# Optimization experiments

Measured on AMD Instinct MI355X. Metric: run time of the kernel, lower is better.

## Reference

```python
import jax, jax.numpy as jnp
import numpy as np

HID = 512; HH = HID // 2; INP = 1; OUT = 1
INH = int(HID * 0.3); EXC = HID - INH            # 153 / 359
N = 3 * HH + 2 * HID + INP                       # 1793 total units
ALM_EXC_START = 3 * HH + HID                      # start of ALM excitatory block
T_CONST = 0.1; SIGMA_REC = 0.01
B, T = 128, 300


def _np_masks():
    rng = np.random.default_rng(0)
    n_zeros = int(np.ceil(0.9 * HH))
    sparse = np.ones((HH, HH), np.float32)
    for c in range(HH):
        sparse[rng.permutation(HH)[:n_zeros], c] = 0.0
    alm2str = np.concatenate([np.ones((HH, EXC), np.float32), np.zeros((HH, INH), np.float32)], 1)
    thal2d1 = np.concatenate([np.ones((HH // 2, HID), np.float32), np.zeros((HH // 2, HID), np.float32)], 0)
    alm2d1 = 1.0 - thal2d1
    iti2d1 = np.concatenate([np.ones((HH // 2, INP), np.float32), np.zeros((HH // 2, INP), np.float32)], 0)
    alm_sign = np.concatenate([np.ones(EXC, np.float32), -np.ones(INH, np.float32)])  # alm2alm_D diagonal
    return sparse, alm2str, thal2d1, alm2d1, iti2d1, alm_sign

_SPARSE, _ALM2STR, _THAL2D1M, _ALM2D1M, _ITI2D1M, _ALMSIGN = [jnp.asarray(a) for a in _np_masks()]


def _clip(w):
    return jnp.clip(w, 1e-10, 1.0)               # F.hardtanh(w, 1e-10, 1)


def _build_W(d12d1_w, d12d2_w, d22d1_w, d22d2_w, d22stn_w, d12thal_w, stn2thal_w,
             thal2alm_w, alm2alm_w, thal2d1_w, thal2d2_w, alm2d1_w, alm2d2_w,
             inp_w_d1, inp_w_d2):
    z_ss = jnp.zeros((HH, HH)); z_sl = jnp.zeros((HH, HID))
    z_ls = jnp.zeros((HID, HH)); z_ll = jnp.zeros((HID, HID))
    z_si = jnp.zeros((HH, INP)); z_li = jnp.zeros((HID, INP))
    # striatal recurrence: sparse_mask * hardtanh(w) @ (-I)
    d12d1 = -(_SPARSE * _clip(d12d1_w)); d12d2 = -(_SPARSE * _clip(d12d2_w))
    d22d1 = -(_SPARSE * _clip(d22d1_w)); d22d2 = -(_SPARSE * _clip(d22d2_w))
    row_d1 = jnp.concatenate([d12d1, d22d1, z_ss, _THAL2D1M * _clip(thal2d1_w),
                              _ALM2D1M * _ALM2STR * _clip(alm2d1_w), _ITI2D1M * _clip(inp_w_d1)], 1)
    row_d2 = jnp.concatenate([d12d2, d22d2, z_ss, _clip(thal2d2_w),
                              _ALM2STR * _clip(alm2d2_w), _clip(inp_w_d2)], 1)
    row_stn = jnp.concatenate([z_ss, _clip(d22stn_w), z_ss, z_sl, z_sl, z_si], 1)
    row_thal = jnp.concatenate([_clip(d12thal_w), z_ls, -_clip(stn2thal_w), z_ll, z_ll, z_li], 1)  # stn2thal @ (-I)
    row_alm = jnp.concatenate([z_ls, z_ls, z_ls, _clip(thal2alm_w),
                               _clip(alm2alm_w) * _ALMSIGN[None, :], z_li], 1)      # alm2alm @ D (Dale)
    row_iti = jnp.zeros((INP, N))
    return jnp.concatenate([row_d1, row_d2, row_stn, row_thal, row_alm, row_iti], 0)


def setup_inputs() -> dict:
    key = jax.random.key(0)
    ks = jax.random.split(key, 24)
    u = lambda k, s: jax.random.uniform(k, s, jnp.float32) * 0.01   # uniform(0, 0.01) init
    return {
        "inp": jax.random.uniform(ks[0], (B, T, INP), jnp.float32),
        "cue_inp": jax.random.uniform(ks[1], (B, T, INP), jnp.float32),
        "inhib_stim": jnp.zeros((B, T, N), jnp.float32),
        "hn": jax.random.uniform(ks[2], (1, B, N), jnp.float32),
        "xn": jax.random.uniform(ks[3], (1, B, N), jnp.float32),
        "noise": jax.random.normal(ks[4], (B, T, N), jnp.float32),
        "d12d1_w": u(ks[5], (HH, HH)), "d12d2_w": u(ks[6], (HH, HH)),
        "d22d1_w": u(ks[7], (HH, HH)), "d22d2_w": u(ks[8], (HH, HH)),
        "d22stn_w": u(ks[9], (HH, HH)), "d12thal_w": u(ks[10], (HID, HH)),
        "stn2thal_w": u(ks[11], (HID, HH)), "thal2alm_w": u(ks[12], (HID, HID)),
        "alm2alm_w": u(ks[13], (HID, HID)), "thal2d1_w": u(ks[14], (HH, HID)),
        "thal2d2_w": u(ks[15], (HH, HID)), "alm2d1_w": u(ks[16], (HH, HID)),
        "alm2d2_w": u(ks[17], (HH, HID)), "inp_w_d1": u(ks[18], (HH, INP)),
        "inp_w_d2": u(ks[19], (HH, INP)), "out_w_alm": u(ks[20], (OUT, EXC)),
    }


def reference(inp, cue_inp, inhib_stim, hn, xn, noise,
              d12d1_w, d12d2_w, d22d1_w, d22d2_w, d22stn_w, d12thal_w, stn2thal_w,
              thal2alm_w, alm2alm_w, thal2d1_w, thal2d2_w, alm2d1_w, alm2d2_w,
              inp_w_d1, inp_w_d2, out_w_alm):
    W = _build_W(d12d1_w, d12d2_w, d22d1_w, d22d2_w, d22stn_w, d12thal_w, stn2thal_w,
                 thal2alm_w, alm2alm_w, thal2d1_w, thal2d2_w, alm2d1_w, alm2d2_w,
                 inp_w_d1, inp_w_d2)
    # tonic current: 0.1 everywhere except ITI units
    tonic = jnp.concatenate([0.1 * jnp.ones(N - INP, jnp.float32), jnp.zeros(INP, jnp.float32)])
    seq = (inhib_stim.swapaxes(0, 1),                 # [T, B, N]
           (inp + cue_inp).swapaxes(0, 1),            # [T, B, INP] -> injected into ITI units
           noise.swapaxes(0, 1))                      # [T, B, N]

    def step(carry, s):
        x, h = carry
        inh_t, iti_t, noise_t = s
        drive = h @ W.T + tonic + inh_t + SIGMA_REC * noise_t
        drive = drive.at[:, N - INP:].add(iti_t)
        x = x + T_CONST * (-x + drive)
        h = jax.nn.relu(x)
        out = h[:, ALM_EXC_START:ALM_EXC_START + EXC] @ out_w_alm.T
        return (x, h), (h, x, out)

    (_, _), (hs, xs, outs) = jax.lax.scan(step, (xn[0], hn[0]), seq)
    return hs.swapaxes(0, 1), xs.swapaxes(0, 1), outs.swapaxes(0, 1)
```

## Files before the change

### kernel.cpp

```cpp
#include <hip/hip_runtime.h>
#include <stdint.h>
#include <string.h>

#define NREAL 1793
#define NPAD  1824
#define NROWP 1808
#define WSTR  1832
#define NBLK  113
#define NGRP  2
#define TSTEPS 300
#define BATCH 128
#define XS_OFF 68851200
#define OUT_OFF 137702400
#define LOFF (16 * WSTR)
#define LOSCALE 4096.0f
#define LOINV  2.44140625e-4f

#define ASLOT(g,i)    (((g) * 128 + (i)) * 32)

typedef _Float16 half_t;
typedef __attribute__((ext_vector_type(8))) _Float16 half8;
typedef __attribute__((ext_vector_type(4))) float f32x4;
typedef __attribute__((ext_vector_type(4))) unsigned int uint4v;

__device__ __forceinline__ float clipw(float w) {
  return fminf(fmaxf(w, 1e-10f), 1.0f);
}

__device__ __forceinline__ void store_u32_llc(unsigned int* p, unsigned int v) {
  asm volatile("global_store_dword %0, %1, off sc0 sc1"
               :: "v"((unsigned long long)(uintptr_t)p), "v"(v)
               : "memory");
}

__device__ __forceinline__ float unpack_h(uint32_t p) {
  unsigned short uh = (unsigned short)(p & 0xffffu);
  unsigned short ul = (unsigned short)(p >> 16);
  half_t hh = *(half_t*)&uh;
  half_t hl = *(half_t*)&ul;
  return (float)hh + LOINV * (float)hl;
}

template<int LO0, int N0, int LO1, int N1, int LO2, int N2>
__device__ __forceinline__ void seg_mfma(const uint32_t* __restrict__ ap,
                                         const half_t* __restrict__ Wl, int wl_b,
                                         f32x4& acc0, f32x4& acc1, f32x4& acc2)
{
  constexpr int NC = N0 + N1 + N2;
  if (NC == 0) return;
  uint4v q0[NC ? NC : 1], q1[NC ? NC : 1];
  #pragma unroll
  for (int i = 0; i < NC; ++i) {
    const int kc = (i < N0) ? (LO0 + i)
                 : (i < N0 + N1) ? (LO1 + i - N0)
                 : (LO2 + i - N0 - N1);
    q0[i] = *(const uint4v*)(ap + kc * 32);
    q1[i] = *(const uint4v*)(ap + kc * 32 + 4);
  }
  #pragma unroll
  for (int i = 0; i < NC; ++i) {
    const int kc = (i < N0) ? (LO0 + i)
                 : (i < N0 + N1) ? (LO1 + i - N0)
                 : (LO2 + i - N0 - N1);
    uint4v uh, ul;
    uh.x = __builtin_amdgcn_perm(q0[i].y, q0[i].x, 0x05040100u);
    uh.y = __builtin_amdgcn_perm(q0[i].w, q0[i].z, 0x05040100u);
    uh.z = __builtin_amdgcn_perm(q1[i].y, q1[i].x, 0x05040100u);
    uh.w = __builtin_amdgcn_perm(q1[i].w, q1[i].z, 0x05040100u);
    ul.x = __builtin_amdgcn_perm(q0[i].y, q0[i].x, 0x07060302u);
    ul.y = __builtin_amdgcn_perm(q0[i].w, q0[i].z, 0x07060302u);
    ul.z = __builtin_amdgcn_perm(q1[i].y, q1[i].x, 0x07060302u);
    ul.w = __builtin_amdgcn_perm(q1[i].w, q1[i].z, 0x07060302u);
    union { uint4v u; half8 h; } ch, cl;
    ch.u = uh; cl.u = ul;
    half8 bvh = *(const half8*)&Wl[wl_b + kc * 32];
    half8 bvl = *(const half8*)&Wl[LOFF + wl_b + kc * 32];
    acc0 = __builtin_amdgcn_mfma_f32_16x16x32_f16(ch.h, bvh, acc0, 0, 0, 0);
    acc1 = __builtin_amdgcn_mfma_f32_16x16x32_f16(ch.h, bvl, acc1, 0, 0, 0);
    acc2 = __builtin_amdgcn_mfma_f32_16x16x32_f16(cl.h, bvh, acc2, 0, 0, 0);
  }
}

__global__ __launch_bounds__(256)
void build_w(const float* __restrict__ d12d1, const float* __restrict__ d12d2,
             const float* __restrict__ d22d1, const float* __restrict__ d22d2,
             const float* __restrict__ d22stn, const float* __restrict__ d12thal,
             const float* __restrict__ stn2thal, const float* __restrict__ thal2alm,
             const float* __restrict__ alm2alm, const float* __restrict__ thal2d1,
             const float* __restrict__ thal2d2, const float* __restrict__ alm2d1,
             const float* __restrict__ alm2d2, const float* __restrict__ inpw1,
             const float* __restrict__ inpw2, const unsigned int* __restrict__ mbits,
             half_t* __restrict__ W)
{
  int idx = blockIdx.x * 256 + threadIdx.x;
  if (idx >= NROWP * NPAD) return;
  int i = idx / NPAD, j = idx - (idx / NPAD) * NPAD;
  float v = 0.f;
  if (i < NREAL && j < NREAL) {
    if (i < 256) {
      if (j < 512) {
        int jj = j & 255;
        unsigned bit = (mbits[(i << 3) + (jj >> 5)] >> (jj & 31)) & 1u;
        float wv = (j < 256) ? d12d1[(i << 8) + jj] : d22d1[(i << 8) + jj];
        v = bit ? -clipw(wv) : 0.f;
      } else if (j < 768) {
      } else if (j < 1280) {
        if (i < 128) v = clipw(thal2d1[(i << 9) + (j - 768)]);
      } else if (j < 1792) {
        int jj = j - 1280;
        if (i >= 128 && jj < 359) v = clipw(alm2d1[(i << 9) + jj]);
      } else {
        if (i < 128) v = clipw(inpw1[i]);
      }
    } else if (i < 512) {
      int ii = i - 256;
      if (j < 512) {
        int jj = j & 255;
        unsigned bit = (mbits[(ii << 3) + (jj >> 5)] >> (jj & 31)) & 1u;
        float wv = (j < 256) ? d12d2[(ii << 8) + jj] : d22d2[(ii << 8) + jj];
        v = bit ? -clipw(wv) : 0.f;
      } else if (j < 768) {
      } else if (j < 1280) {
        v = clipw(thal2d2[(ii << 9) + (j - 768)]);
      } else if (j < 1792) {
        int jj = j - 1280;
        if (jj < 359) v = clipw(alm2d2[(ii << 9) + jj]);
      } else {
        v = clipw(inpw2[ii]);
      }
    } else if (i < 768) {
      int ii = i - 512;
      if (j >= 256 && j < 512) v = clipw(d22stn[(ii << 8) + (j - 256)]);
    } else if (i < 1280) {
      int ii = i - 768;
      if (j < 256) v = clipw(d12thal[(ii << 8) + j]);
      else if (j >= 512 && j < 768) v = -clipw(stn2thal[(ii << 8) + (j - 512)]);
    } else if (i < 1792) {
      int ii = i - 1280;
      if (j >= 768 && j < 1280) v = clipw(thal2alm[(ii << 9) + (j - 768)]);
      else if (j >= 1280) {
        int jj = j - 1280;
        v = clipw(alm2alm[(ii << 9) + jj]) * ((jj < 359) ? 1.f : -1.f);
      }
    }
  }
  half_t vh = (half_t)v;
  half_t vl = (half_t)((v - (float)vh) * LOSCALE);
  W[idx] = vh;
  W[(size_t)NROWP * NPAD + idx] = vl;
}

__global__ __launch_bounds__(256)
void init_h(const float* __restrict__ hn, uint32_t* __restrict__ hbuf)
{
  const size_t P4 = (size_t)BATCH * NPAD;
  int idx = blockIdx.x * 256 + threadIdx.x;
  if (idx >= BATCH * NPAD) return;
  int b = idx / NPAD, k = idx - b * NPAD;
  float v = (k < NREAL) ? hn[b * NREAL + k] : 0.f;
  half_t vh = (half_t)v;
  half_t vl = (half_t)((v - (float)vh) * LOSCALE);
  uint32_t hp = (uint32_t)(*(unsigned short*)&vh) |
                ((uint32_t)(*(unsigned short*)&vl) << 16);
  hbuf[idx]      = hp;
  hbuf[P4 + idx] = 0u;
}

__global__ __launch_bounds__(256, 1)
void rnn_step_all(const half_t* __restrict__ Wg, uint32_t* __restrict__ hbuf,
                  unsigned int* __restrict__ cnt,
                  const float* __restrict__ inp, const float* __restrict__ cue,
                  const float* __restrict__ inhib, const float* __restrict__ noise,
                  const float* __restrict__ xn, const float* __restrict__ outw,
                  float* __restrict__ dout)
{
  __shared__ __align__(16) half_t Wl[2 * 16 * WSTR];
  const int tid = threadIdx.x;
  const int bid = blockIdx.x;
  const int g  = bid / NBLK;
  const int nb = bid - g * NBLK;
  const int r0 = nb * 16;
  const int bg = g * 64;
  const size_t P4 = (size_t)BATCH * NPAD;

  const int lane = tid & 63;
  const int w    = tid >> 6;
  const int n_i  = lane & 15;
  const int kq   = lane >> 4;
  const int row  = r0 + n_i;
  const bool valid = row < NREAL;
  const int b0 = bg + 16 * w + kq * 4;
  const int bA = bg + 16 * w + n_i;
  const int wl_b = n_i * WSTR + kq * 8;
  const bool is_outblk = (r0 == 512);
  const bool poll_wave = (tid < 64);

  float inh[4], noi[4];
  #pragma unroll
  for (int r = 0; r < 4; ++r) {
    inh[r] = 0.f; noi[r] = 0.f;
    if (valid) {
      int ei = ((b0 + r) * TSTEPS) * NREAL + row;
      inh[r] = __builtin_nontemporal_load(&inhib[ei]);
      noi[r] = __builtin_nontemporal_load(&noise[ei]);
    }
  }

  for (int idx = tid; idx < 2 * 16 * (NPAD / 8); idx += 256) {
    int p   = idx / (16 * (NPAD / 8));
    int rem = idx - p * 16 * (NPAD / 8);
    int rr  = rem / (NPAD / 8);
    int cc  = (rem - rr * (NPAD / 8)) * 8;
    *(uint4v*)&Wl[p * LOFF + rr * WSTR + cc] =
        *(const uint4v*)&Wg[(size_t)p * NROWP * NPAD + (size_t)(r0 + rr) * NPAD + cc];
  }
  __syncthreads();

  float xr[4];
  #pragma unroll
  for (int r = 0; r < 4; ++r)
    xr[r] = valid ? xn[(size_t)(b0 + r) * NREAL + row] : 0.f;

  const float tonic = (valid && row < 1792) ? 0.1f : 0.f;
  const bool is_iti = (row == 1792);

  const int ob    = bg + 16 * w + (lane >> 2);
  const int opart = lane & 3;
  const int ou0   = opart * 90;
  const int onu   = (opart == 3) ? 89 : 90;

  #pragma unroll 1
  for (int t = 0; t < TSTEPS; ++t) {
    const uint32_t* hr = hbuf + (size_t)(t & 1) * P4;
    uint32_t*       hw = hbuf + (size_t)((t & 1) ^ 1) * P4;

    float itv[4];
    #pragma unroll
    for (int r = 0; r < 4; ++r) {
      int bt = (b0 + r) * TSTEPS + t;
      itv[r] = is_iti ? (inp[bt] + cue[bt]) : 0.f;
    }

    const uint32_t* ap = hr + (size_t)bA * NPAD + kq * 8;
    f32x4 acc0 = {0.f, 0.f, 0.f, 0.f};
    f32x4 acc1 = {0.f, 0.f, 0.f, 0.f};
    f32x4 acc2 = {0.f, 0.f, 0.f, 0.f};

    if      (r0 < 128)  seg_mfma<0, 16, 24, 16, 56, 1>(ap, Wl, wl_b, acc0, acc1, acc2);
    else if (r0 < 256)  seg_mfma<0, 16, 40, 12,  0, 0>(ap, Wl, wl_b, acc0, acc1, acc2);
    else if (r0 < 512)  seg_mfma<0, 16, 24, 28, 56, 1>(ap, Wl, wl_b, acc0, acc1, acc2);
    else if (r0 < 768)  seg_mfma<8,  8,  0,  0,  0, 0>(ap, Wl, wl_b, acc0, acc1, acc2);
    else if (r0 < 1280) seg_mfma<0,  8, 16,  8,  0, 0>(ap, Wl, wl_b, acc0, acc1, acc2);
    else if (r0 < 1792) seg_mfma<24, 32, 0,  0,  0, 0>(ap, Wl, wl_b, acc0, acc1, acc2);

    #pragma unroll
    for (int r = 0; r < 4; ++r) {
      float drive = acc0[r] + LOINV * (acc1[r] + acc2[r])
                    + tonic + inh[r] + 0.01f * noi[r] + itv[r];
      float xv = xr[r] + 0.1f * (drive - xr[r]);
      float hv = fmaxf(xv, 0.f);
      xr[r] = xv;
      int bt = (b0 + r) * TSTEPS + t;
      if (valid) {
        int ei = bt * NREAL + row;
        __builtin_nontemporal_store(hv, &dout[ei]);
        __builtin_nontemporal_store(xv, &dout[XS_OFF + ei]);
      }
      half_t hh = (half_t)hv;
      half_t hl = (half_t)((hv - (float)hh) * LOSCALE);
      uint32_t hp = (uint32_t)(*(unsigned short*)&hh) |
                    ((uint32_t)(*(unsigned short*)&hl) << 16);
      store_u32_llc(&hw[(size_t)(b0 + r) * NPAD + row], hp);
    }

    if (is_outblk && t >= 1) {
      const uint32_t* hb = hr + (size_t)ob * NPAD + 1280 + ou0;
      float s = 0.f;
      #pragma unroll 10
      for (int i = 0; i < onu; ++i)
        s += unpack_h(hb[i]) * outw[ou0 + i];
      s += __shfl_xor(s, 1);
      s += __shfl_xor(s, 2);
      if (opart == 0)
        __builtin_nontemporal_store(s, &dout[OUT_OFF + ob * TSTEPS + (t - 1)]);
    }

    if (t + 1 < TSTEPS) {
      #pragma unroll
      for (int r = 0; r < 4; ++r) {
        if (valid) {
          int ei = ((b0 + r) * TSTEPS + (t + 1)) * NREAL + row;
          inh[r] = __builtin_nontemporal_load(&inhib[ei]);
          noi[r] = __builtin_nontemporal_load(&noise[ei]);
        }
      }
      const unsigned epoch = (unsigned)(t + 1);
      asm volatile("s_waitcnt vmcnt(8)" ::: "memory");
      __builtin_amdgcn_s_barrier();
      if (tid == 0)
        store_u32_llc(&cnt[ASLOT(g, nb)], epoch);
      if (poll_wave) {
        unsigned m;
        for (;;) {
          unsigned v0 = __hip_atomic_load(&cnt[ASLOT(g, lane)],
                                          __ATOMIC_RELAXED, __HIP_MEMORY_SCOPE_AGENT);
          unsigned v1 = 0xFFFFFFFFu;
          if (lane + 64 < NBLK)
            v1 = __hip_atomic_load(&cnt[ASLOT(g, lane + 64)],
                                   __ATOMIC_RELAXED, __HIP_MEMORY_SCOPE_AGENT);
          m = v0 < v1 ? v0 : v1;
          #pragma unroll
          for (int o = 32; o; o >>= 1) {
            unsigned mo = __shfl_xor(m, o);
            m = m < mo ? m : mo;
          }
          if (m >= epoch) break;
          __builtin_amdgcn_s_sleep(1);
        }
        __builtin_amdgcn_fence(__ATOMIC_ACQUIRE, "agent");
        asm volatile("s_waitcnt vmcnt(0)" ::: "memory");
      }
      __builtin_amdgcn_s_barrier();
    }
  }

  asm volatile("s_waitcnt vmcnt(0)" ::: "memory");
  __builtin_amdgcn_s_barrier();
  if (tid == 0)
    store_u32_llc(&cnt[ASLOT(g, nb)], (unsigned)TSTEPS);
  if (is_outblk) {
    if (poll_wave) {
      unsigned m;
      for (;;) {
        unsigned v0 = __hip_atomic_load(&cnt[ASLOT(g, lane)],
                                        __ATOMIC_RELAXED, __HIP_MEMORY_SCOPE_AGENT);
        unsigned v1 = 0xFFFFFFFFu;
        if (lane + 64 < NBLK)
          v1 = __hip_atomic_load(&cnt[ASLOT(g, lane + 64)],
                                 __ATOMIC_RELAXED, __HIP_MEMORY_SCOPE_AGENT);
        m = v0 < v1 ? v0 : v1;
        #pragma unroll
        for (int o = 32; o; o >>= 1) {
          unsigned mo = __shfl_xor(m, o);
          m = m < mo ? m : mo;
        }
        if (m >= (unsigned)TSTEPS) break;
        __builtin_amdgcn_s_sleep(1);
      }
      __builtin_amdgcn_fence(__ATOMIC_ACQUIRE, "agent");
      asm volatile("s_waitcnt vmcnt(0)" ::: "memory");
    }
    __builtin_amdgcn_s_barrier();
    const uint32_t* hr = hbuf + (size_t)(TSTEPS & 1) * P4;
    const uint32_t* hb = hr + (size_t)ob * NPAD + 1280 + ou0;
    float s = 0.f;
    #pragma unroll 10
    for (int i = 0; i < onu; ++i)
      s += unpack_h(hb[i]) * outw[ou0 + i];
    s += __shfl_xor(s, 1);
    s += __shfl_xor(s, 2);
    if (opart == 0)
      __builtin_nontemporal_store(s, &dout[OUT_OFF + ob * TSTEPS + (TSTEPS - 1)]);
  }
}

static void compute_sparse_mask(uint32_t* mb) {
  uint32_t pool[4];
  uint32_t hc = 0x43b0d7e5u;
  auto hashmix = [&hc](uint32_t value) -> uint32_t {
    value ^= hc; hc *= 0x931e8875u; value *= hc; value ^= value >> 16; return value;
  };
  auto mixf = [](uint32_t x, uint32_t y) -> uint32_t {
    uint32_t r = x * 0xca01f9ddu;
    r -= y * 0x4973f715u;
    r ^= r >> 16;
    return r;
  };
  for (int i = 0; i < 4; ++i) pool[i] = hashmix(0u);
  for (int s = 0; s < 4; ++s)
    for (int d = 0; d < 4; ++d)
      if (s != d) pool[d] = mixf(pool[d], hashmix(pool[s]));
  uint32_t st[8];
  uint32_t hb = 0x8b51f9ddu;
  for (int i = 0; i < 8; ++i) {
    uint32_t dv = pool[i & 3];
    dv ^= hb; hb *= 0x58f38dedu; dv *= hb; dv ^= dv >> 16;
    st[i] = dv;
  }
  uint64_t v64[4];
  for (int i = 0; i < 4; ++i) v64[i] = (uint64_t)st[2 * i] | ((uint64_t)st[2 * i + 1] << 32);
  typedef unsigned __int128 u128;
  const u128 MULT = ((u128)0x2360ed051fc65da4ULL << 64) | 0x4385df649fccf645ULL;
  u128 initstate = ((u128)v64[0] << 64) | v64[1];
  u128 initseq   = ((u128)v64[2] << 64) | v64[3];
  u128 state = 0, inc = (initseq << 1) | 1;
  state = state * MULT + inc;
  state += initstate;
  state = state * MULT + inc;
  bool has32 = false; uint32_t cached = 0;
  auto next64 = [&]() -> uint64_t {
    state = state * MULT + inc;
    uint64_t hi = (uint64_t)(state >> 64), lo = (uint64_t)state;
    unsigned rot = (unsigned)(state >> 122);
    uint64_t x = hi ^ lo;
    return (x >> rot) | (x << ((64 - rot) & 63));
  };
  auto next32 = [&]() -> uint32_t {
    if (has32) { has32 = false; return cached; }
    uint64_t v = next64();
    has32 = true; cached = (uint32_t)(v >> 32);
    return (uint32_t)v;
  };
  auto rinterval = [&](uint32_t mx) -> uint32_t {
    if (mx == 0) return 0;
    uint32_t mask = mx;
    mask |= mask >> 1; mask |= mask >> 2; mask |= mask >> 4;
    mask |= mask >> 8; mask |= mask >> 16;
    uint32_t value;
    do { value = next32() & mask; } while (value > mx);
    return value;
  };
  for (int i = 0; i < 256 * 8; ++i) mb[i] = 0xFFFFFFFFu;
  int perm[256];
  for (int c = 0; c < 256; ++c) {
    for (int i = 0; i < 256; ++i) perm[i] = i;
    for (int i = 255; i >= 1; --i) {
      uint32_t j = rinterval((uint32_t)i);
      int tmp = perm[i]; perm[i] = perm[j]; perm[j] = tmp;
    }
    for (int z = 0; z < 231; ++z)
      mb[perm[z] * 8 + (c >> 5)] &= ~(1u << (c & 31));
  }
}

extern "C" void kernel_launch(void* const* d_in, const int* in_sizes, int n_in,
                              void* d_out, int out_size, void* d_ws, size_t ws_size,
                              hipStream_t stream)
{
  (void)in_sizes; (void)n_in; (void)out_size; (void)ws_size;
  const float* inp   = (const float*)d_in[0];
  const float* cue   = (const float*)d_in[1];
  const float* inhib = (const float*)d_in[2];
  const float* hn    = (const float*)d_in[3];
  const float* xn    = (const float*)d_in[4];
  const float* noise = (const float*)d_in[5];
  const float* outw  = (const float*)d_in[21];
  float* dout = (float*)d_out;

  char* ws = (char*)d_ws;
  const size_t W_BYTES = (size_t)2 * NROWP * NPAD * sizeof(half_t);
  const size_t H_BYTES = (size_t)2 * BATCH * NPAD * 4;
  half_t*   W    = (half_t*)ws;
  uint32_t* hbuf = (uint32_t*)(ws + W_BYTES);
  unsigned int* mbits = (unsigned int*)(ws + W_BYTES + H_BYTES);
  unsigned int* cnt   = (unsigned int*)(ws + W_BYTES + H_BYTES + 32768);

  static uint32_t hmask[256 * 8];
  compute_sparse_mask(hmask);
  (void)hipMemcpyAsync(mbits, hmask, sizeof(hmask), hipMemcpyHostToDevice, stream);
  (void)hipMemsetAsync(cnt, 0, 32768, stream);

  build_w<<<(NROWP * NPAD + 255) / 256, 256, 0, stream>>>(
      (const float*)d_in[6],  (const float*)d_in[7],  (const float*)d_in[8],
      (const float*)d_in[9],  (const float*)d_in[10], (const float*)d_in[11],
      (const float*)d_in[12], (const float*)d_in[13], (const float*)d_in[14],
      (const float*)d_in[15], (const float*)d_in[16], (const float*)d_in[17],
      (const float*)d_in[18], (const float*)d_in[19], (const float*)d_in[20],
      mbits, W);
  init_h<<<(BATCH * NPAD + 255) / 256, 256, 0, stream>>>(hn, hbuf);

  void* args[] = {(void*)&W, (void*)&hbuf, (void*)&cnt, (void*)&inp, (void*)&cue,
                  (void*)&inhib, (void*)&noise, (void*)&xn, (void*)&outw, (void*)&dout};
  hipError_t err = hipLaunchCooperativeKernel(reinterpret_cast<void*>(rnn_step_all),
                                              dim3(NGRP * NBLK), dim3(256), args, 0, stream);
  if (err != hipSuccess) {
    rnn_step_all<<<dim3(NGRP * NBLK), dim3(256), 0, stream>>>(
        W, hbuf, cnt, inp, cue, inhib, noise, xn, outw, dout);
  }
}
```

Measured before the change: 4.143 ms.

## Replace global per-step barrier with dependency-aware point-to-point waits and quad buffering

Each block now waits only on the row-region blocks whose outputs its sparse weight segments actually read. It also waits on consumers being at most two steps behind, rather than on all blocks in the group every step. The h state buffer goes from double to quad buffering so producers can run ahead without overwriting data still being read. This cuts time lost to the global barrier and skew between blocks, at the cost of more workspace and hand-coded dependency bitmasks that must match the segment layout exactly.

Measured after the change: 3.902 ms. 5.8% less time.

```diff
diff --git a/kernel.cpp b/kernel.cpp
--- a/kernel.cpp
+++ b/kernel.cpp
@@ -39,6 +39,37 @@
   half_t hh = *(half_t*)&uh;
   half_t hl = *(half_t*)&ul;
   return (float)hh + LOINV * (float)hl;
+}
+
+__device__ __forceinline__ int rid_of(int s) {
+  return (s < 8) ? 0 : (s < 16) ? 1 : (s < 32) ? 2 : (s < 48) ? 3
+       : (s < 80) ? 4 : (s < 112) ? 5 : 6;
+}
+
+__device__ __forceinline__ void poll_wait(unsigned int* cnt, int g, int lane,
+                                          bool in0, bool in1, bool cn0, bool cn1,
+                                          unsigned tin, unsigned tcn)
+{
+  const int s0 = lane, s1 = lane + 64;
+  for (;;) {
+    unsigned a0 = __hip_atomic_load(&cnt[ASLOT(g, s0)], __ATOMIC_RELAXED,
+                                    __HIP_MEMORY_SCOPE_AGENT);
+    unsigned a1 = 0xFFFFFFFFu;
+    if (in1 || cn1)
+      a1 = __hip_atomic_load(&cnt[ASLOT(g, s1)], __ATOMIC_RELAXED,
+                             __HIP_MEMORY_SCOPE_AGENT);
+    unsigned vin = in0 ? a0 : 0xFFFFFFFFu;
+    if (in1 && a1 < vin) vin = a1;
+    unsigned vcn = cn0 ? a0 : 0xFFFFFFFFu;
+    if (cn1 && a1 < vcn) vcn = a1;
+    #pragma unroll
+    for (int o = 32; o; o >>= 1) {
+      unsigned x = __shfl_xor(vin, o); if (x < vin) vin = x;
+      unsigned y = __shfl_xor(vcn, o); if (y < vcn) vcn = y;
+    }
+    if (vin >= tin && vcn >= tcn) break;
+    __builtin_amdgcn_s_sleep(1);
+  }
 }
 
 template<int LO0, int N0, int LO1, int N1, int LO2, int N2>
@@ -195,6 +226,22 @@
   const bool is_outblk = (r0 == 512);
   const bool poll_wave = (tid < 64);
 
+  const int myrid = rid_of(nb);
+  const unsigned INB =
+      (myrid == 0) ? 87u : (myrid == 1) ? 39u : (myrid == 2) ? 119u :
+      (myrid == 3) ? ((nb == 32) ? 36u : 4u) :
+      (myrid == 4) ? 11u : (myrid == 5) ? 48u : 0u;
+  const unsigned CONSB =
+      (myrid <= 1) ? 23u : (myrid == 2) ? 15u : (myrid == 3) ? 16u :
+      (myrid == 4) ? 37u : (myrid == 5) ? 46u : 5u;
+  const int s1 = lane + 64;
+  const int rid0 = rid_of(lane);
+  const int rid1 = (s1 < NBLK) ? rid_of(s1) : 6;
+  const bool in0 = (lane != nb) && ((INB >> rid0) & 1);
+  const bool in1 = (s1 < NBLK) && (s1 != nb) && ((INB >> rid1) & 1);
+  const bool cn0 = ((CONSB >> rid0) & 1);
+  const bool cn1 = (s1 < NBLK) && ((CONSB >> rid1) & 1);
+
   float inh[4], noi[4];
   #pragma unroll
   for (int r = 0; r < 4; ++r) {
@@ -231,8 +278,19 @@
 
   #pragma unroll 1
   for (int t = 0; t < TSTEPS; ++t) {
-    const uint32_t* hr = hbuf + (size_t)(t & 1) * P4;
-    uint32_t*       hw = hbuf + (size_t)((t & 1) ^ 1) * P4;
+    if (t >= 1) {
+      if (poll_wave) {
+        poll_wait(cnt, g, lane, in0, in1, cn0, cn1,
+                  (unsigned)t, (t >= 2) ? (unsigned)(t - 2) : 0u);
+        __builtin_amdgcn_fence(__ATOMIC_ACQUIRE, "agent");
+        asm volatile("s_waitcnt vmcnt(0)" ::: "memory");
+      }
+      __builtin_amdgcn_s_barrier();
+      asm volatile("" ::: "memory");
+    }
+
+    const uint32_t* hr = hbuf + (size_t)(t & 3) * P4;
+    uint32_t*       hw = hbuf + (size_t)((t + 1) & 3) * P4;
 
     float itv[4];
     #pragma unroll
@@ -294,64 +352,24 @@
           noi[r] = __builtin_nontemporal_load(&noise[ei]);
         }
       }
-      const unsigned epoch = (unsigned)(t + 1);
       asm volatile("s_waitcnt vmcnt(8)" ::: "memory");
-      __builtin_amdgcn_s_barrier();
-      if (tid == 0)
-        store_u32_llc(&cnt[ASLOT(g, nb)], epoch);
-      if (poll_wave) {
-        unsigned m;
-        for (;;) {
-          unsigned v0 = __hip_atomic_load(&cnt[ASLOT(g, lane)],
-                                          __ATOMIC_RELAXED, __HIP_MEMORY_SCOPE_AGENT);
-          unsigned v1 = 0xFFFFFFFFu;
-          if (lane + 64 < NBLK)
-            v1 = __hip_atomic_load(&cnt[ASLOT(g, lane + 64)],
-                                   __ATOMIC_RELAXED, __HIP_MEMORY_SCOPE_AGENT);
-          m = v0 < v1 ? v0 : v1;
-          #pragma unroll
-          for (int o = 32; o; o >>= 1) {
-            unsigned mo = __shfl_xor(m, o);
-            m = m < mo ? m : mo;
-          }
-          if (m >= epoch) break;
-          __builtin_amdgcn_s_sleep(1);
-        }
-        __builtin_amdgcn_fence(__ATOMIC_ACQUIRE, "agent");
-        asm volatile("s_waitcnt vmcnt(0)" ::: "memory");
-      }
-      __builtin_amdgcn_s_barrier();
-    }
-  }
-
-  asm volatile("s_waitcnt vmcnt(0)" ::: "memory");
-  __builtin_amdgcn_s_barrier();
-  if (tid == 0)
-    store_u32_llc(&cnt[ASLOT(g, nb)], (unsigned)TSTEPS);
+    } else {
+      asm volatile("s_waitcnt vmcnt(0)" ::: "memory");
+    }
+    __builtin_amdgcn_s_barrier();
+    if (tid == 0)
+      store_u32_llc(&cnt[ASLOT(g, nb)], (unsigned)(t + 1));
+  }
+
   if (is_outblk) {
     if (poll_wave) {
-      unsigned m;
-      for (;;) {
-        unsigned v0 = __hip_atomic_load(&cnt[ASLOT(g, lane)],
-                                        __ATOMIC_RELAXED, __HIP_MEMORY_SCOPE_AGENT);
-        unsigned v1 = 0xFFFFFFFFu;
-        if (lane + 64 < NBLK)
-          v1 = __hip_atomic_load(&cnt[ASLOT(g, lane + 64)],
-                                 __ATOMIC_RELAXED, __HIP_MEMORY_SCOPE_AGENT);
-        m = v0 < v1 ? v0 : v1;
-        #pragma unroll
-        for (int o = 32; o; o >>= 1) {
-          unsigned mo = __shfl_xor(m, o);
-          m = m < mo ? m : mo;
-        }
-        if (m >= (unsigned)TSTEPS) break;
-        __builtin_amdgcn_s_sleep(1);
-      }
+      poll_wait(cnt, g, lane, in0, in1, false, false, (unsigned)TSTEPS, 0u);
       __builtin_amdgcn_fence(__ATOMIC_ACQUIRE, "agent");
       asm volatile("s_waitcnt vmcnt(0)" ::: "memory");
     }
     __builtin_amdgcn_s_barrier();
-    const uint32_t* hr = hbuf + (size_t)(TSTEPS & 1) * P4;
+    asm volatile("" ::: "memory");
+    const uint32_t* hr = hbuf + (size_t)(TSTEPS & 3) * P4;
     const uint32_t* hb = hr + (size_t)ob * NPAD + 1280 + ou0;
     float s = 0.f;
     #pragma unroll 10
@@ -449,7 +467,7 @@
 
   char* ws = (char*)d_ws;
   const size_t W_BYTES = (size_t)2 * NROWP * NPAD * sizeof(half_t);
-  const size_t H_BYTES = (size_t)2 * BATCH * NPAD * 4;
+  const size_t H_BYTES = (size_t)4 * BATCH * NPAD * 4;
   half_t*   W    = (half_t*)ws;
   uint32_t* hbuf = (uint32_t*)(ws + W_BYTES);
   unsigned int* mbits = (unsigned int*)(ws + W_BYTES + H_BYTES);
```
